# Performance work log

Measured on AMD Instinct MI355X. Metric: run time of the kernel, lower is better.

The kernel has to match this reference:

```python
import jax, jax.numpy as jnp
import numpy as np

FORWARD_W = 1.0
BACKWARD_W = 1.0
NORMAL_W = 0.1
EPS = 1e-6


def setup_inputs() -> dict:
    key = jax.random.key(0)
    ks = jax.random.split(key, 5)
    N, M = 8192, 8192
    sp = jax.random.normal(ks[0], (N, 3), dtype=jnp.float32)
    tp = jax.random.normal(ks[1], (M, 3), dtype=jnp.float32)
    sn = jax.random.normal(ks[2], (N, 3), dtype=jnp.float32)
    tn = jax.random.normal(ks[3], (M, 3), dtype=jnp.float32)
    sn = sn / jnp.linalg.norm(sn, axis=1, keepdims=True)
    tn = tn / jnp.linalg.norm(tn, axis=1, keepdims=True)
    rot6d = jnp.array([1.0, 0.05, -0.02, 0.03, 1.0, 0.04], dtype=jnp.float32)
    rot6d = rot6d + 0.01 * jax.random.normal(ks[4], (6,), dtype=jnp.float32)
    return {
        'source_points': sp, 'target_points': tp,
        'source_normals': sn, 'target_normals': tn,
        'translation': jnp.zeros(3, jnp.float32),
        'rotation_6d': rot6d,
        'scale': jnp.ones(3, jnp.float32),
    }


def rotation_6d_to_matrix(r6):
    a1, a2 = r6[:3], r6[3:]
    b1 = a1 / jnp.linalg.norm(a1)
    b2 = a2 - jnp.sum(b1 * a2) * b1
    b2 = b2 / jnp.linalg.norm(b2)
    b3 = jnp.cross(b1, b2)
    return jnp.stack([b1, b2, b3], axis=1)  # (3,3), columns are b1,b2,b3


def cos_sim(a, b):
    na = jnp.maximum(jnp.linalg.norm(a, axis=1), EPS)
    nb = jnp.maximum(jnp.linalg.norm(b, axis=1), EPS)
    return jnp.sum(a * b, axis=1) / (na * nb)


def reference(source_points, target_points, source_normals, target_normals,
              translation, rotation_6d, scale):
    R = rotation_6d_to_matrix(rotation_6d)
    # apply_transformation: scale -> rotate -> translate
    src = (source_points * scale[None, :]) @ R.T + translation[None, :]  # (N,3)
    src_n = source_normals @ R.T  # (N,3)

    # pairwise squared distances (N,M)
    d2 = (jnp.sum(src * src, axis=1)[:, None]
          + jnp.sum(target_points * target_points, axis=1)[None, :]
          - 2.0 * src @ target_points.T)
    d2 = jnp.maximum(d2, 0.0)

    d_s2t = jnp.min(d2, axis=1)          # (N,) squared NN dist source->target
    idx_s = jnp.argmin(d2, axis=1)       # (N,)
    d_t2s = jnp.min(d2, axis=0)          # (M,)
    idx_t = jnp.argmin(d2, axis=0)       # (M,)

    loss = FORWARD_W * jnp.mean(d_s2t) + BACKWARD_W * jnp.mean(d_t2s)

    # normal loss: 1 - |cos| against matched normals (both directions)
    cn_s = 1.0 - jnp.abs(cos_sim(src_n, target_normals[idx_s]))
    cn_t = 1.0 - jnp.abs(cos_sim(target_normals, src_n[idx_t]))
    loss = loss + NORMAL_W * (jnp.mean(cn_s) + jnp.mean(cn_t))
    return loss
```

## Files before the change

### kernel.cpp

```cpp
#include <hip/hip_runtime.h>
#include <math.h>

#define FW 1.0f
#define BW 1.0f
#define NW 0.1f
#define EPSV 1e-6f

#define BT  256
#define MPT 8
#define JCH 128

#define COMPUTE_R(r6)                                                         \
    float a1x = (r6)[0], a1y = (r6)[1], a1z = (r6)[2];                        \
    float a2x = (r6)[3], a2y = (r6)[4], a2z = (r6)[5];                        \
    float n1 = sqrtf(a1x*a1x + a1y*a1y + a1z*a1z);                            \
    float b1x = a1x/n1, b1y = a1y/n1, b1z = a1z/n1;                           \
    float dp = b1x*a2x + b1y*a2y + b1z*a2z;                                   \
    float u2x = a2x - dp*b1x, u2y = a2y - dp*b1y, u2z = a2z - dp*b1z;         \
    float n2 = sqrtf(u2x*u2x + u2y*u2y + u2z*u2z);                            \
    float b2x = u2x/n2, b2y = u2y/n2, b2z = u2z/n2;                           \
    float b3x = b1y*b2z - b1z*b2y;                                            \
    float b3y = b1z*b2x - b1x*b2z;                                            \
    float b3z = b1x*b2y - b1y*b2x;

__global__ __launch_bounds__(BT) void transform_kernel(
    const float* __restrict__ sp, const float* __restrict__ tp,
    const float* __restrict__ sn,
    const float* __restrict__ trans, const float* __restrict__ r6,
    const float* __restrict__ scl,
    float4* __restrict__ src4, float4* __restrict__ tgt4,
    float4* __restrict__ srcn4,
    unsigned long long* __restrict__ min_s,
    unsigned long long* __restrict__ min_t,
    float* __restrict__ out, int N, int M)
{
    int i = blockIdx.x * BT + threadIdx.x;

    if (blockIdx.y == 1) {
        if (i < M) {
            float x = tp[3*i], y = tp[3*i+1], z = tp[3*i+2];
            tgt4[i] = make_float4(x, y, z, x*x + y*y + z*z);
            min_t[i] = ~0ull;
        }
        return;
    }

    if (i == 0) out[0] = 0.f;
    if (i >= N) return;
    min_s[i] = ~0ull;

    COMPUTE_R(r6)

    float qx = sp[3*i]   * scl[0];
    float qy = sp[3*i+1] * scl[1];
    float qz = sp[3*i+2] * scl[2];
    float sx = b1x*qx + b2x*qy + b3x*qz + trans[0];
    float sy = b1y*qx + b2y*qy + b3y*qz + trans[1];
    float sz = b1z*qx + b2z*qy + b3z*qz + trans[2];
    src4[i] = make_float4(sx, sy, sz, sx*sx + sy*sy + sz*sz);

    float nx = sn[3*i], ny = sn[3*i+1], nz = sn[3*i+2];
    srcn4[i] = make_float4(b1x*nx + b2x*ny + b3x*nz,
                           b1y*nx + b2y*ny + b3y*nz,
                           b1z*nx + b2z*ny + b3z*nz, 0.f);
}

__global__ __launch_bounds__(BT) void min_kernel(
    const float4* __restrict__ src4, const float4* __restrict__ tgt4,
    unsigned long long* __restrict__ min_s,
    unsigned long long* __restrict__ min_t, int N, int M)
{
    const float4* A; const float4* B; unsigned long long* outm; int nA, nB;
    if (blockIdx.z == 0) { A = src4; B = tgt4; outm = min_s; nA = N; nB = M; }
    else                 { A = tgt4; B = src4; outm = min_t; nA = M; nB = N; }

    const int tid   = threadIdx.x;
    const int aBase = blockIdx.x * (BT * MPT);
    const int jBase = blockIdx.y * JCH;
    if (aBase >= nA || jBase >= nB) return;

    __shared__ float4 bs[JCH];

    float cx[MPT], cy[MPT], cz[MPT], s2[MPT], best[MPT];
    #pragma unroll
    for (int p = 0; p < MPT; p++) {
        int ia = aBase + p*BT + tid; if (ia >= nA) ia = 0;
        float4 a = A[ia];
        cx[p] = -2.f*a.x; cy[p] = -2.f*a.y; cz[p] = -2.f*a.z;
        s2[p] = a.w;
        best[p] = 3.4e38f;
    }
    if (tid < JCH) {
        int jb = jBase + tid;
        bs[tid] = B[jb < nB ? jb : nB - 1];
    }
    __syncthreads();

    int jLim = nB - jBase; if (jLim > JCH) jLim = JCH;
    #pragma unroll 2
    for (int j = 0; j < jLim; j++) {
        float4 b = bs[j];
        #pragma unroll
        for (int p = 0; p < MPT; p++) {
            float e = fmaf(cz[p], b.z, b.w);
            e = fmaf(cy[p], b.y, e);
            e = fmaf(cx[p], b.x, e);
            float em = __uint_as_float(
                (__float_as_uint(e) & 0xFFFFFF00u) | (unsigned int)j);
            best[p] = fminf(best[p], em);
        }
    }

    #pragma unroll
    for (int p = 0; p < MPT; p++) {
        int ia = aBase + p*BT + tid;
        if (ia < nA) {
            unsigned int eb = __float_as_uint(best[p]);
            int jloc = (int)(eb & 0xFFu);
            float ec = __uint_as_float(eb & 0xFFFFFF00u);
            float d = fmaxf(ec + s2[p], 0.f);
            unsigned long long pk =
                ((unsigned long long)__float_as_uint(d) << 32) |
                (unsigned int)(jBase + jloc);
            atomicMin(&outm[ia], pk);
        }
    }
}

__global__ __launch_bounds__(BT) void reduce_kernel(
    const unsigned long long* __restrict__ min_s,
    const unsigned long long* __restrict__ min_t,
    const float4* __restrict__ srcn4, const float* __restrict__ tn,
    float* __restrict__ out, int N, int M)
{
    int gid = blockIdx.x * BT + threadIdx.x;
    float contrib = 0.f;

    if (gid < N) {
        unsigned long long pk = min_s[gid];
        float d = __uint_as_float((unsigned int)(pk >> 32));
        int idx = (int)(unsigned int)(pk & 0xffffffffull);
        float4 nv = srcn4[gid];
        float tx = tn[3*idx], ty = tn[3*idx+1], tz = tn[3*idx+2];
        float na = fmaxf(sqrtf(nv.x*nv.x + nv.y*nv.y + nv.z*nv.z), EPSV);
        float nb = fmaxf(sqrtf(tx*tx + ty*ty + tz*tz), EPSV);
        float cs = (nv.x*tx + nv.y*ty + nv.z*tz) / (na * nb);
        contrib = (FW * d + NW * (1.f - fabsf(cs))) * (1.f / N);
    } else if (gid < N + M) {
        int j = gid - N;
        unsigned long long pk = min_t[j];
        float d = __uint_as_float((unsigned int)(pk >> 32));
        int idx = (int)(unsigned int)(pk & 0xffffffffull);
        float tx = tn[3*j], ty = tn[3*j+1], tz = tn[3*j+2];
        float4 nv = srcn4[idx];
        float na = fmaxf(sqrtf(tx*tx + ty*ty + tz*tz), EPSV);
        float nb = fmaxf(sqrtf(nv.x*nv.x + nv.y*nv.y + nv.z*nv.z), EPSV);
        float cs = (tx*nv.x + ty*nv.y + tz*nv.z) / (na * nb);
        contrib = (BW * d + NW * (1.f - fabsf(cs))) * (1.f / M);
    }

    #pragma unroll
    for (int o = 32; o > 0; o >>= 1)
        contrib += __shfl_down(contrib, o, 64);

    __shared__ float wsum[BT/64];
    if ((threadIdx.x & 63) == 0) wsum[threadIdx.x >> 6] = contrib;
    __syncthreads();
    if (threadIdx.x == 0) {
        float s = 0.f;
        #pragma unroll
        for (int w = 0; w < BT/64; w++) s += wsum[w];
        atomicAdd(out, s);
    }
}

extern "C" void kernel_launch(void* const* d_in, const int* in_sizes, int n_in,
                              void* d_out, int out_size, void* d_ws, size_t ws_size,
                              hipStream_t stream) {
    const float* sp    = (const float*)d_in[0];
    const float* tp    = (const float*)d_in[1];
    const float* sn    = (const float*)d_in[2];
    const float* tn    = (const float*)d_in[3];
    const float* trans = (const float*)d_in[4];
    const float* r6    = (const float*)d_in[5];
    const float* scl   = (const float*)d_in[6];
    float* out = (float*)d_out;

    const int N = in_sizes[0] / 3;
    const int M = in_sizes[1] / 3;

    char* ws = (char*)d_ws;
    float4* src4  = (float4*)(ws);
    float4* tgt4  = (float4*)(ws + (size_t)16*N);
    float4* srcn4 = (float4*)(ws + (size_t)16*N + (size_t)16*M);
    unsigned long long* min_s =
        (unsigned long long*)(ws + (size_t)32*N + (size_t)16*M);
    unsigned long long* min_t = min_s + N;

    int nmax = N > M ? N : M;
    dim3 tgrid((nmax + BT - 1) / BT, 2);
    transform_kernel<<<tgrid, BT, 0, stream>>>(sp, tp, sn, trans, r6, scl,
                                               src4, tgt4, srcn4,
                                               min_s, min_t, out, N, M);

    dim3 mgrid((nmax + BT*MPT - 1) / (BT*MPT), (nmax + JCH - 1) / JCH, 2);
    min_kernel<<<mgrid, BT, 0, stream>>>(src4, tgt4, min_s, min_t, N, M);

    int rblocks = (N + M + BT - 1) / BT;
    reduce_kernel<<<rblocks, BT, 0, stream>>>(min_s, min_t, srcn4, tn, out, N, M);
}
```

Before: 89.77 us.

## Track winning chunk only in min kernel, recover exact argmin in reduce

The inner distance loop no longer packs the local index into the low mantissa bits, which drops an and/or pair per candidate. The atomicMin payload now records only the winning chunk index. The reduce kernel rescans that 128-element chunk to recover the exact argmin and distance before computing the normal terms. This moves a small per-point rescan into the reduce pass in exchange for a leaner hot loop, and it also avoids the precision loss from truncated mantissas.

```diff
diff --git a/kernel.cpp b/kernel.cpp
--- a/kernel.cpp
+++ b/kernel.cpp
@@ -105,9 +105,7 @@
             float e = fmaf(cz[p], b.z, b.w);
             e = fmaf(cy[p], b.y, e);
             e = fmaf(cx[p], b.x, e);
-            float em = __uint_as_float(
-                (__float_as_uint(e) & 0xFFFFFF00u) | (unsigned int)j);
-            best[p] = fminf(best[p], em);
+            best[p] = fminf(best[p], e);
         }
     }
 
@@ -115,13 +113,10 @@
     for (int p = 0; p < MPT; p++) {
         int ia = aBase + p*BT + tid;
         if (ia < nA) {
-            unsigned int eb = __float_as_uint(best[p]);
-            int jloc = (int)(eb & 0xFFu);
-            float ec = __uint_as_float(eb & 0xFFFFFF00u);
-            float d = fmaxf(ec + s2[p], 0.f);
+            float d = fmaxf(best[p] + s2[p], 0.f);
             unsigned long long pk =
                 ((unsigned long long)__float_as_uint(d) << 32) |
-                (unsigned int)(jBase + jloc);
+                (unsigned int)blockIdx.y;
             atomicMin(&outm[ia], pk);
         }
     }
@@ -130,33 +125,57 @@
 __global__ __launch_bounds__(BT) void reduce_kernel(
     const unsigned long long* __restrict__ min_s,
     const unsigned long long* __restrict__ min_t,
+    const float4* __restrict__ src4, const float4* __restrict__ tgt4,
     const float4* __restrict__ srcn4, const float* __restrict__ tn,
     float* __restrict__ out, int N, int M)
 {
     int gid = blockIdx.x * BT + threadIdx.x;
     float contrib = 0.f;
 
-    if (gid < N) {
-        unsigned long long pk = min_s[gid];
-        float d = __uint_as_float((unsigned int)(pk >> 32));
-        int idx = (int)(unsigned int)(pk & 0xffffffffull);
-        float4 nv = srcn4[gid];
-        float tx = tn[3*idx], ty = tn[3*idx+1], tz = tn[3*idx+2];
-        float na = fmaxf(sqrtf(nv.x*nv.x + nv.y*nv.y + nv.z*nv.z), EPSV);
-        float nb = fmaxf(sqrtf(tx*tx + ty*ty + tz*tz), EPSV);
-        float cs = (nv.x*tx + nv.y*ty + nv.z*tz) / (na * nb);
-        contrib = (FW * d + NW * (1.f - fabsf(cs))) * (1.f / N);
-    } else if (gid < N + M) {
-        int j = gid - N;
-        unsigned long long pk = min_t[j];
-        float d = __uint_as_float((unsigned int)(pk >> 32));
-        int idx = (int)(unsigned int)(pk & 0xffffffffull);
-        float tx = tn[3*j], ty = tn[3*j+1], tz = tn[3*j+2];
-        float4 nv = srcn4[idx];
-        float na = fmaxf(sqrtf(tx*tx + ty*ty + tz*tz), EPSV);
-        float nb = fmaxf(sqrtf(nv.x*nv.x + nv.y*nv.y + nv.z*nv.z), EPSV);
-        float cs = (tx*nv.x + ty*nv.y + tz*nv.z) / (na * nb);
-        contrib = (BW * d + NW * (1.f - fabsf(cs))) * (1.f / M);
+    if (gid < N + M) {
+        const int dir = (gid < N) ? 0 : 1;
+        const int i   = dir ? (gid - N) : gid;
+        const float4* Ap = dir ? tgt4 : src4;
+        const float4* Bp = dir ? src4 : tgt4;
+        const int nB  = dir ? N : M;
+        unsigned long long pk = dir ? min_t[i] : min_s[i];
+
+        const int jBase = (int)(unsigned int)(pk & 0xffffffffull) * JCH;
+        int jLim = nB - jBase; if (jLim > JCH) jLim = JCH;
+
+        float4 a = Ap[i];
+        float cx = -2.f*a.x, cy = -2.f*a.y, cz = -2.f*a.z;
+
+        float bestE = 3.4e38f; int bestJ = 0;
+        const float4* bp = Bp + jBase;
+        #pragma unroll 4
+        for (int j = 0; j < jLim; j++) {
+            float4 b = bp[j];
+            float e = fmaf(cz, b.z, b.w);
+            e = fmaf(cy, b.y, e);
+            e = fmaf(cx, b.x, e);
+            bool c = e < bestE;
+            bestE = c ? e : bestE;
+            bestJ = c ? j : bestJ;
+        }
+        float d = fmaxf(bestE + a.w, 0.f);
+        int idx = jBase + bestJ;
+
+        if (dir == 0) {
+            float4 nv = srcn4[i];
+            float tx = tn[3*idx], ty = tn[3*idx+1], tz = tn[3*idx+2];
+            float na = fmaxf(sqrtf(nv.x*nv.x + nv.y*nv.y + nv.z*nv.z), EPSV);
+            float nb = fmaxf(sqrtf(tx*tx + ty*ty + tz*tz), EPSV);
+            float cs = (nv.x*tx + nv.y*ty + nv.z*tz) / (na * nb);
+            contrib = (FW * d + NW * (1.f - fabsf(cs))) * (1.f / N);
+        } else {
+            float tx = tn[3*i], ty = tn[3*i+1], tz = tn[3*i+2];
+            float4 nv = srcn4[idx];
+            float na = fmaxf(sqrtf(tx*tx + ty*ty + tz*tz), EPSV);
+            float nb = fmaxf(sqrtf(nv.x*nv.x + nv.y*nv.y + nv.z*nv.z), EPSV);
+            float cs = (tx*nv.x + ty*nv.y + tz*nv.z) / (na * nb);
+            contrib = (BW * d + NW * (1.f - fabsf(cs))) * (1.f / M);
+        }
     }
 
     #pragma unroll
@@ -207,5 +226,6 @@
     min_kernel<<<mgrid, BT, 0, stream>>>(src4, tgt4, min_s, min_t, N, M);
 
     int rblocks = (N + M + BT - 1) / BT;
-    reduce_kernel<<<rblocks, BT, 0, stream>>>(min_s, min_t, srcn4, tn, out, N, M);
-}
+    reduce_kernel<<<rblocks, BT, 0, stream>>>(min_s, min_t, src4, tgt4,
+                                              srcn4, tn, out, N, M);
+}
```

Measured after the change: 99.44 us. 1.11x slower.
